# Performance work log

Hardware: AMD Instinct MI355X
Metric: run time of the kernel (lower is better)

## Reference

```python
import jax, jax.numpy as jnp
import numpy as np

TEMP = 0.5
ALPHA, BETA, GAMMA, LAMB = 1e-3, 5e-4, 1e-3, 5e-6
IMG = 1024.0  # img_metas img_shape (H_img, W_img)
LN_EPS = 1e-5


def setup_inputs() -> dict:
    key = jax.random.key(0)
    ks = jax.random.split(key, 20)
    N, C, H, W, NB = 8, 256, 128, 128, 20
    preds_S = jax.random.normal(ks[0], (N, C, H, W), jnp.float32)
    preds_T = jax.random.normal(ks[1], (N, C, H, W), jnp.float32)
    # valid boxes (tl_x, tl_y, br_x, br_y) in pixel coords within [0, IMG]
    raw = jax.random.uniform(ks[2], (N, NB, 4), jnp.float32)
    x1 = raw[..., 0] * 0.7 * IMG
    y1 = raw[..., 1] * 0.7 * IMG
    x2 = jnp.minimum(x1 + (0.05 + raw[..., 2] * 0.25) * IMG, IMG)
    y2 = jnp.minimum(y1 + (0.05 + raw[..., 3] * 0.25) * IMG, IMG)
    gt_bboxes = jnp.stack([x1, y1, x2, y2], axis=-1)
    s = 1.0 / np.sqrt(C)
    s2 = 1.0 / np.sqrt(C // 2)
    mk = lambda k, shape, sc: jax.random.normal(k, shape, jnp.float32) * sc
    return {
        'preds_S': preds_S, 'preds_T': preds_T, 'gt_bboxes': gt_bboxes,
        'w_ms': mk(ks[3], (C,), s), 'b_ms': jnp.zeros((), jnp.float32),
        'w_mt': mk(ks[4], (C,), s), 'b_mt': jnp.zeros((), jnp.float32),
        'w1_s': mk(ks[5], (C // 2, C), s), 'b1_s': jnp.zeros((C // 2,), jnp.float32),
        'g_s': jnp.ones((C // 2,), jnp.float32), 'be_s': jnp.zeros((C // 2,), jnp.float32),
        'w2_s': mk(ks[6], (C, C // 2), s2), 'b2_s': jnp.zeros((C,), jnp.float32),
        'w1_t': mk(ks[7], (C // 2, C), s), 'b1_t': jnp.zeros((C // 2,), jnp.float32),
        'g_t': jnp.ones((C // 2,), jnp.float32), 'be_t': jnp.zeros((C // 2,), jnp.float32),
        'w2_t': mk(ks[8], (C, C // 2), s2), 'b2_t': jnp.zeros((C,), jnp.float32),
    }


def _attention(x):
    # x: [N,C,H,W] -> S_att [N,H,W], C_att [N,C]
    N, C, H, W = x.shape
    v = jnp.abs(x)
    fea = v.mean(axis=1)                                   # [N,H,W]
    S = (H * W) * jax.nn.softmax((fea / TEMP).reshape(N, -1), axis=1)
    ch = v.mean(axis=(2, 3))                               # [N,C]
    Ca = C * jax.nn.softmax(ch / TEMP, axis=1)
    return S.reshape(N, H, W), Ca


def _masks(gt, H, W):
    # gt: [N,nb,4] pixel coords; box-rasterized scatter-max foreground mask
    wmin = jnp.floor(gt[..., 0] / IMG * W)
    wmax = jnp.ceil(gt[..., 2] / IMG * W)
    hmin = jnp.floor(gt[..., 1] / IMG * H)
    hmax = jnp.ceil(gt[..., 3] / IMG * H)
    area = 1.0 / ((hmax + 1.0 - hmin) * (wmax + 1.0 - wmin))  # [N,nb]
    hs = jnp.arange(H, dtype=jnp.float32)[None, None, :, None]
    ws = jnp.arange(W, dtype=jnp.float32)[None, None, None, :]
    inb = (hs >= hmin[:, :, None, None]) & (hs <= hmax[:, :, None, None]) \
        & (ws >= wmin[:, :, None, None]) & (ws <= wmax[:, :, None, None])
    Mask_fg = jnp.where(inb, area[:, :, None, None], 0.0).max(axis=1)  # [N,H,W]
    Mask_bg = jnp.where(Mask_fg > 0, 0.0, 1.0)
    sbg = Mask_bg.sum(axis=(1, 2), keepdims=True)
    Mask_bg = jnp.where(sbg > 0, Mask_bg / sbg, Mask_bg)
    return Mask_fg, Mask_bg


def _spatial_pool(x, w, b):
    N, C, H, W = x.shape
    cm = jnp.einsum('nchw,c->nhw', x, w) + b
    sm = jax.nn.softmax(cm.reshape(N, -1), axis=1).reshape(N, H, W)
    return jnp.einsum('nchw,nhw->nc', x, sm)               # [N,C]


def _channel_add(ctx, w1, b1, g, be, w2, b2):
    y = ctx @ w1.T + b1                                    # [N,C/2]
    m = y.mean(axis=1, keepdims=True)
    v = y.var(axis=1, keepdims=True)
    y = (y - m) / jnp.sqrt(v + LN_EPS) * g + be
    y = jax.nn.relu(y)
    return y @ w2.T + b2                                   # [N,C]


def reference(preds_S, preds_T, gt_bboxes, w_ms, b_ms, w_mt, b_mt,
              w1_s, b1_s, g_s, be_s, w2_s, b2_s,
              w1_t, b1_t, g_t, be_t, w2_t, b2_t):
    N, C, H, W = preds_S.shape
    S_t, C_t = _attention(preds_T)
    S_s, C_s = _attention(preds_S)
    Mask_fg, Mask_bg = _masks(gt_bboxes, H, W)
    # feature losses: (fg_s - fg_t) = (S - T) * sqrt(S_t)*sqrt(C_t)*sqrt(mask)
    wgt = jnp.sqrt(S_t)[:, None] * jnp.sqrt(C_t)[:, :, None, None]
    d = (preds_S - preds_T) * wgt
    fg_loss = jnp.sum((d * jnp.sqrt(Mask_fg)[:, None]) ** 2) / N
    bg_loss = jnp.sum((d * jnp.sqrt(Mask_bg)[:, None]) ** 2) / N
    mask_loss = jnp.sum(jnp.abs(C_s - C_t)) / N + jnp.sum(jnp.abs(S_s - S_t)) / N
    ctx_s = _spatial_pool(preds_S, w_ms, b_ms)
    ctx_t = _spatial_pool(preds_T, w_mt, b_mt)
    add_s = _channel_add(ctx_s, w1_s, b1_s, g_s, be_s, w2_s, b2_s)
    add_t = _channel_add(ctx_t, w1_t, b1_t, g_t, be_t, w2_t, b2_t)
    rd = (preds_S + add_s[:, :, None, None]) - (preds_T + add_t[:, :, None, None])
    rela_loss = jnp.sum(rd ** 2) / N
    return ALPHA * fg_loss + BETA * bg_loss + GAMMA * mask_loss + LAMB * rela_loss
```

## Files before the change

kernel.cpp:

```cpp
#include <hip/hip_runtime.h>
#include <math.h>

#define NN    8
#define CC    256
#define HWHW  16384
#define NBOX  20

constexpr float C_ALPHA = 1e-3f, C_BETA = 5e-4f, C_GAMMA = 1e-3f, C_LAMB = 5e-6f;
constexpr float C_LN_EPS = 1e-5f;

#define OFF_FEA_S   0
#define OFF_FEA_T   131072
#define OFF_CM_S    262144
#define OFF_CM_T    393216
#define OFF_MFG     524288
#define OFF_PCHS    655360
#define OFF_PCHT    786432
#define OFF_PD      917504
#define OFF_PCTXS   1048576
#define OFF_PCTXT   1179648
#define OFF_CATT    1310720
#define OFF_CTXS    1312768
#define OFF_CTXT    1314816
#define OFF_DSUM    1316864
#define OFF_STATS   1318912
#define OFF_MXP     1318976
#define OFF_ZP      1319488
#define OFF_BG      1320000
#define OFF_SCAL    1320008
#define OFF_Y       1320016
#define OFF_RELAP   1322064

__device__ __forceinline__ float dpp_wave_sum(float x) {
#define DPPADD(ctrl, rm) \
  x += __int_as_float(__builtin_amdgcn_update_dpp(0, __float_as_int(x), ctrl, rm, 0xf, true));
  DPPADD(0x111, 0xf)
  DPPADD(0x112, 0xf)
  DPPADD(0x114, 0xf)
  DPPADD(0x118, 0xf)
  DPPADD(0x142, 0xa)
  DPPADD(0x143, 0xc)
#undef DPPADD
  return x;
}

__device__ __forceinline__ float dpp_wave_max(float x) {
#define DPPMAX(ctrl, rm) { \
  int r_ = __builtin_amdgcn_update_dpp(__float_as_int(x), __float_as_int(x), ctrl, rm, 0xf, false); \
  x = fmaxf(x, __int_as_float(r_)); }
  DPPMAX(0x111, 0xf)
  DPPMAX(0x112, 0xf)
  DPPMAX(0x114, 0xf)
  DPPMAX(0x118, 0xf)
  DPPMAX(0x142, 0xa)
  DPPMAX(0x143, 0xc)
#undef DPPMAX
  return x;
}

__device__ __forceinline__ float block_sum256(float v, float* sm) {
  int tid = threadIdx.x;
  v = dpp_wave_sum(v);
  if ((tid & 63) == 63) sm[tid >> 6] = v;
  __syncthreads();
  float r = sm[0] + sm[1] + sm[2] + sm[3];
  __syncthreads();
  return r;
}

__device__ __forceinline__ float block_max256(float v, float* sm) {
  int tid = threadIdx.x;
  v = dpp_wave_max(v);
  if ((tid & 63) == 63) sm[tid >> 6] = v;
  __syncthreads();
  float r = fmaxf(fmaxf(sm[0], sm[1]), fmaxf(sm[2], sm[3]));
  __syncthreads();
  return r;
}

__global__ __launch_bounds__(512, 8) void k1_pass1(
    const float* __restrict__ S, const float* __restrict__ T,
    const float* __restrict__ w_ms, const float* __restrict__ w_mt,
    float* __restrict__ ws) {
  int tid = threadIdx.x;
  int lane = tid & 63, sl = tid >> 6;
  int pb = blockIdx.x, cs = blockIdx.y, n = blockIdx.z;
  int pix0 = pb * 256 + lane * 4;
  int ch0 = cs * 128 + sl * 16;

  __shared__ float l_wS[128], l_wT[128];
  __shared__ float f_feaS[256], f_feaT[256], f_cmS[256], f_cmT[256];
  __shared__ float l_chS[128], l_chT[128], l_D[128];
  __shared__ float l_sq[8];

  if (tid < 128) {
    l_wS[tid] = w_ms[cs * 128 + tid];
    l_wT[tid] = w_mt[cs * 128 + tid];
  }
  if (tid < 256) {
    f_feaS[tid] = 0.f; f_feaT[tid] = 0.f; f_cmS[tid] = 0.f; f_cmT[tid] = 0.f;
  }
  __syncthreads();

  const float* baseS = S + (size_t)(n * CC + ch0) * HWHW + pix0;
  const float* baseT = T + (size_t)(n * CC + ch0) * HWHW + pix0;

  float fSx = 0, fSy = 0, fSz = 0, fSw = 0;
  float fTx = 0, fTy = 0, fTz = 0, fTw = 0;
  float cSx = 0, cSy = 0, cSz = 0, cSw = 0;
  float cTx = 0, cTy = 0, cTz = 0, cTw = 0;
  float sq = 0.f;

#pragma unroll 2
  for (int c = 0; c < 16; c++) {
    float4 s4 = *(const float4*)(baseS + (size_t)c * HWHW);
    float4 t4 = *(const float4*)(baseT + (size_t)c * HWHW);
    float asx = fabsf(s4.x), asy = fabsf(s4.y), asz = fabsf(s4.z), asw = fabsf(s4.w);
    float atx = fabsf(t4.x), aty = fabsf(t4.y), atz = fabsf(t4.z), atw = fabsf(t4.w);
    fSx += asx; fSy += asy; fSz += asz; fSw += asw;
    fTx += atx; fTy += aty; fTz += atz; fTw += atw;
    float wS = l_wS[sl * 16 + c], wT = l_wT[sl * 16 + c];
    cSx = fmaf(s4.x, wS, cSx); cSy = fmaf(s4.y, wS, cSy);
    cSz = fmaf(s4.z, wS, cSz); cSw = fmaf(s4.w, wS, cSw);
    cTx = fmaf(t4.x, wT, cTx); cTy = fmaf(t4.y, wT, cTy);
    cTz = fmaf(t4.z, wT, cTz); cTw = fmaf(t4.w, wT, cTw);
    float dx = s4.x - t4.x, dy = s4.y - t4.y, dz = s4.z - t4.z, dw = s4.w - t4.w;
    sq = fmaf(dx, dx, sq); sq = fmaf(dy, dy, sq);
    sq = fmaf(dz, dz, sq); sq = fmaf(dw, dw, sq);
    float chS_p = (asx + asy) + (asz + asw);
    float chT_p = (atx + aty) + (atz + atw);
    float d_p   = (dx + dy) + (dz + dw);
    chS_p = dpp_wave_sum(chS_p);
    chT_p = dpp_wave_sum(chT_p);
    d_p   = dpp_wave_sum(d_p);
    if (lane == 63) {
      l_chS[sl * 16 + c] = chS_p;
      l_chT[sl * 16 + c] = chT_p;
      l_D[sl * 16 + c]   = d_p;
    }
  }

  atomicAdd(&f_feaS[lane * 4 + 0], fSx); atomicAdd(&f_feaS[lane * 4 + 1], fSy);
  atomicAdd(&f_feaS[lane * 4 + 2], fSz); atomicAdd(&f_feaS[lane * 4 + 3], fSw);
  atomicAdd(&f_feaT[lane * 4 + 0], fTx); atomicAdd(&f_feaT[lane * 4 + 1], fTy);
  atomicAdd(&f_feaT[lane * 4 + 2], fTz); atomicAdd(&f_feaT[lane * 4 + 3], fTw);
  atomicAdd(&f_cmS[lane * 4 + 0], cSx); atomicAdd(&f_cmS[lane * 4 + 1], cSy);
  atomicAdd(&f_cmS[lane * 4 + 2], cSz); atomicAdd(&f_cmS[lane * 4 + 3], cSw);
  atomicAdd(&f_cmT[lane * 4 + 0], cTx); atomicAdd(&f_cmT[lane * 4 + 1], cTy);
  atomicAdd(&f_cmT[lane * 4 + 2], cTz); atomicAdd(&f_cmT[lane * 4 + 3], cTw);

  sq = dpp_wave_sum(sq);
  if (lane == 63) l_sq[sl] = sq;
  __syncthreads();

  if (tid < 256) {
    int gp = n * HWHW + pb * 256 + tid;
    atomicAdd(&ws[OFF_FEA_S + gp], f_feaS[tid]);
    atomicAdd(&ws[OFF_FEA_T + gp], f_feaT[tid]);
    atomicAdd(&ws[OFF_CM_S + gp],  f_cmS[tid]);
    atomicAdd(&ws[OFF_CM_T + gp],  f_cmT[tid]);
  }
  if (tid < 128) {
    int bo = (n * CC + cs * 128 + tid) * 64 + pb;
    ws[OFF_PCHS + bo] = l_chS[tid];
    ws[OFF_PCHT + bo] = l_chT[tid];
    ws[OFF_PD + bo]   = l_D[tid];
  }
  if (tid == 0) {
    float t = 0.f;
#pragma unroll
    for (int i = 0; i < 8; i++) t += l_sq[i];
    atomicAdd(&ws[OFF_SCAL + 0], t);
  }
}

__global__ __launch_bounds__(256) void k2_mask(const float* __restrict__ gt,
                                               float* __restrict__ ws) {
  int tid = threadIdx.x;
  int n   = blockIdx.x >> 6;
  int pix = ((blockIdx.x & 63) << 8) | tid;
  float hf = (float)(pix >> 7), wf = (float)(pix & 127);

  __shared__ float bx[NBOX][5];
  __shared__ float l_bg[4];
  if (tid < NBOX) {
    const float* g = gt + (n * NBOX + tid) * 4;
    float wmin = floorf(g[0] * 0.125f);
    float hmin = floorf(g[1] * 0.125f);
    float wmax = ceilf(g[2] * 0.125f);
    float hmax = ceilf(g[3] * 0.125f);
    bx[tid][0] = wmin; bx[tid][1] = hmin; bx[tid][2] = wmax; bx[tid][3] = hmax;
    bx[tid][4] = 1.0f / ((hmax + 1.0f - hmin) * (wmax + 1.0f - wmin));
  }
  __syncthreads();

  float best = 0.f;
#pragma unroll
  for (int b = 0; b < NBOX; b++) {
    bool in = (hf >= bx[b][1]) && (hf <= bx[b][3]) && (wf >= bx[b][0]) && (wf <= bx[b][2]);
    best = in ? fmaxf(best, bx[b][4]) : best;
  }
  ws[OFF_MFG + n * HWHW + pix] = best;

  float bg = (best > 0.f) ? 0.f : 1.f;
  bg = dpp_wave_sum(bg);
  if ((tid & 63) == 63) l_bg[tid >> 6] = bg;
  __syncthreads();
  if (tid == 0) atomicAdd(&ws[OFF_BG + n], l_bg[0] + l_bg[1] + l_bg[2] + l_bg[3]);
}

__global__ __launch_bounds__(256) void kB_stats1(float* __restrict__ ws) {
  int tid = threadIdx.x;
  int pb = blockIdx.x, n = blockIdx.y;
  __shared__ float sm[4];
  int pix0 = pb * 1024 + tid * 4;
  const int   offs[4]   = {OFF_FEA_S, OFF_FEA_T, OFF_CM_S, OFF_CM_T};
  const float scales[4] = {1.0f / 128.0f, 1.0f / 128.0f, 1.0f, 1.0f};
#pragma unroll
  for (int a = 0; a < 4; a++) {
    float4 v = *(const float4*)&ws[offs[a] + n * HWHW + pix0];
    float sc = scales[a];
    v.x *= sc; v.y *= sc; v.z *= sc; v.w *= sc;
    float mx = fmaxf(fmaxf(v.x, v.y), fmaxf(v.z, v.w));
    mx = block_max256(mx, sm);
    float z = expf(v.x - mx) + expf(v.y - mx) + expf(v.z - mx) + expf(v.w - mx);
    z = block_sum256(z, sm);
    if (tid == 0) {
      ws[OFF_MXP + a * 128 + n * 16 + pb] = mx;
      ws[OFF_ZP + a * 128 + n * 16 + pb]  = z;
    }
  }
}

__global__ __launch_bounds__(256) void kC_stats2(float* __restrict__ ws) {
  int tid = threadIdx.x, n = blockIdx.x;
  __shared__ float sm[4];

  float chS = 0.f, chT = 0.f, Dv = 0.f;
  int base = (n * CC + tid) * 64;
#pragma unroll 4
  for (int k = 0; k < 64; k += 4) {
    float4 a = *(const float4*)&ws[OFF_PCHS + base + k];
    float4 b = *(const float4*)&ws[OFF_PCHT + base + k];
    float4 d = *(const float4*)&ws[OFF_PD + base + k];
    chS += (a.x + a.y) + (a.z + a.w);
    chT += (b.x + b.y) + (b.z + b.w);
    Dv  += (d.x + d.y) + (d.z + d.w);
  }
  ws[OFF_DSUM + n * CC + tid] = Dv;

  float lS = chS * (1.0f / 8192.0f), lT = chT * (1.0f / 8192.0f);
  float mS = block_max256(lS, sm);
  float mT = block_max256(lT, sm);
  float eS = expf(lS - mS), eT = expf(lT - mT);
  float ZS = block_sum256(eS, sm);
  float ZT = block_sum256(eT, sm);
  float cattS = (float)CC * eS / ZS;
  float cattT = (float)CC * eT / ZT;
  ws[OFF_CATT + n * CC + tid] = cattT;
  float mml = block_sum256(fabsf(cattS - cattT), sm);
  if (tid == 0) atomicAdd(&ws[OFF_SCAL + 2], mml);

  if (tid < 4) {
    int a = tid;
    float m = -1e30f;
    for (int i = 0; i < 16; i++)
      m = fmaxf(m, ws[OFF_MXP + a * 128 + n * 16 + i]);
    float Z = 0.f;
    for (int i = 0; i < 16; i++)
      Z += ws[OFF_ZP + a * 128 + n * 16 + i] *
           expf(ws[OFF_MXP + a * 128 + n * 16 + i] - m);
    ws[OFF_STATS + n * 8 + 2 * a]     = m;
    ws[OFF_STATS + n * 8 + 2 * a + 1] = Z;
  }
}

__global__ __launch_bounds__(512, 8) void k4_pass2(
    const float* __restrict__ S, const float* __restrict__ T,
    float* __restrict__ ws) {
  int tid = threadIdx.x;
  int lane = tid & 63, sl = tid >> 6;
  int pb = blockIdx.x, cs = blockIdx.y, n = blockIdx.z;
  int pix0 = pb * 256 + lane * 4;
  int ch0 = cs * 128 + sl * 16;

  __shared__ float l_catt[128];
  __shared__ float wcombL[256], smsL[256], smtL[256];
  __shared__ float l_cs[128], l_ct[128], l_c[8];

  if (tid < 128) l_catt[tid] = ws[OFF_CATT + n * CC + cs * 128 + tid];
  if (tid < 64) {
    float mxFS = ws[OFF_STATS + n * 8 + 0], ZFS = ws[OFF_STATS + n * 8 + 1];
    float mxFT = ws[OFF_STATS + n * 8 + 2], ZFT = ws[OFF_STATS + n * 8 + 3];
    float mxCS = ws[OFF_STATS + n * 8 + 4], ZCS = ws[OFF_STATS + n * 8 + 5];
    float mxCT = ws[OFF_STATS + n * 8 + 6], ZCT = ws[OFF_STATS + n * 8 + 7];
    float bgc  = ws[OFF_BG + n];
    int gp = n * HWHW + pb * 256 + tid * 4;
    float4 fS = *(const float4*)&ws[OFF_FEA_S + gp];
    float4 fT = *(const float4*)&ws[OFF_FEA_T + gp];
    float4 cS = *(const float4*)&ws[OFF_CM_S + gp];
    float4 cT = *(const float4*)&ws[OFF_CM_T + gp];
    float4 mf = *(const float4*)&ws[OFF_MFG + gp];
    float macc = 0.f;
    float fSa[4] = {fS.x, fS.y, fS.z, fS.w};
    float fTa[4] = {fT.x, fT.y, fT.z, fT.w};
    float cSa[4] = {cS.x, cS.y, cS.z, cS.w};
    float cTa[4] = {cT.x, cT.y, cT.z, cT.w};
    float mfa[4] = {mf.x, mf.y, mf.z, mf.w};
#pragma unroll
    for (int j = 0; j < 4; j++) {
      float pT = expf(fTa[j] * (1.0f / 128.0f) - mxFT) / ZFT;
      float pS = expf(fSa[j] * (1.0f / 128.0f) - mxFS) / ZFS;
      float Satt = (float)HWHW * pT;
      float mbg = (mfa[j] > 0.f) ? 0.f : ((bgc > 0.f) ? 1.0f / bgc : 1.0f);
      wcombL[tid * 4 + j] = Satt * (C_ALPHA * mfa[j] + C_BETA * mbg);
      smsL[tid * 4 + j] = expf(cSa[j] - mxCS) / ZCS;
      smtL[tid * 4 + j] = expf(cTa[j] - mxCT) / ZCT;
      macc += fabsf(pS - pT);
    }
    macc = dpp_wave_sum(macc);
    if (tid == 63 && cs == 0) atomicAdd(&ws[OFF_SCAL + 2], macc * (float)HWHW);
  }
  __syncthreads();

  float4 sms = *(const float4*)&smsL[lane * 4];
  float4 smt = *(const float4*)&smtL[lane * 4];
  float4 wcb = *(const float4*)&wcombL[lane * 4];

  const float* baseS = S + (size_t)(n * CC + ch0) * HWHW + pix0;
  const float* baseT = T + (size_t)(n * CC + ch0) * HWHW + pix0;

  float awx = 0, awy = 0, awz = 0, aww = 0;
#pragma unroll 2
  for (int c = 0; c < 16; c++) {
    float4 s4 = *(const float4*)(baseS + (size_t)c * HWHW);
    float4 t4 = *(const float4*)(baseT + (size_t)c * HWHW);
    float ca = l_catt[sl * 16 + c];
    float dx = s4.x - t4.x, dy = s4.y - t4.y, dz = s4.z - t4.z, dw = s4.w - t4.w;
    awx = fmaf(dx * dx, ca, awx); awy = fmaf(dy * dy, ca, awy);
    awz = fmaf(dz * dz, ca, awz); aww = fmaf(dw * dw, ca, aww);
    float xs = fmaf(s4.x, sms.x, fmaf(s4.y, sms.y, fmaf(s4.z, sms.z, s4.w * sms.w)));
    float xt = fmaf(t4.x, smt.x, fmaf(t4.y, smt.y, fmaf(t4.z, smt.z, t4.w * smt.w)));
    xs = dpp_wave_sum(xs);
    xt = dpp_wave_sum(xt);
    if (lane == 63) { l_cs[sl * 16 + c] = xs; l_ct[sl * 16 + c] = xt; }
  }

  float contrib = fmaf(awx, wcb.x, fmaf(awy, wcb.y, fmaf(awz, wcb.z, aww * wcb.w)));
  contrib = dpp_wave_sum(contrib);
  if (lane == 63) l_c[sl] = contrib;
  __syncthreads();

  if (tid < 128) {
    int bo = (n * CC + cs * 128 + tid) * 64 + pb;
    ws[OFF_PCTXS + bo] = l_cs[tid];
    ws[OFF_PCTXT + bo] = l_ct[tid];
  }
  if (tid == 0) {
    float t = 0.f;
#pragma unroll
    for (int i = 0; i < 8; i++) t += l_c[i];
    atomicAdd(&ws[OFF_SCAL + 1], t);
  }
}

__global__ __launch_bounds__(256) void k4b_ctxreduce(float* __restrict__ ws) {
  int tid = threadIdx.x, n = blockIdx.x;
  float a = 0.f, b = 0.f;
  int base = (n * CC + tid) * 64;
#pragma unroll 4
  for (int k = 0; k < 64; k += 4) {
    float4 x = *(const float4*)&ws[OFF_PCTXS + base + k];
    float4 y = *(const float4*)&ws[OFF_PCTXT + base + k];
    a += (x.x + x.y) + (x.z + x.w);
    b += (y.x + y.y) + (y.z + y.w);
  }
  ws[OFF_CTXS + n * CC + tid] = a;
  ws[OFF_CTXT + n * CC + tid] = b;
}

__global__ __launch_bounds__(128) void k5a_mlp1(
    const float* __restrict__ w1_s, const float* __restrict__ b1_s,
    const float* __restrict__ g_s,  const float* __restrict__ be_s,
    const float* __restrict__ w1_t, const float* __restrict__ b1_t,
    const float* __restrict__ g_t,  const float* __restrict__ be_t,
    float* __restrict__ ws) {
  int tid = threadIdx.x;
  int n = blockIdx.x >> 1, st = blockIdx.x & 1;
  const float* w1 = st ? w1_t : w1_s;
  const float* b1 = st ? b1_t : b1_s;
  const float* g  = st ? g_t  : g_s;
  const float* be = st ? be_t : be_s;
  int ctxoff = (st ? OFF_CTXT : OFF_CTXS) + n * CC;

  __shared__ float ctx[CC];
  __shared__ float red[2];
  ctx[tid]       = ws[ctxoff + tid];
  ctx[tid + 128] = ws[ctxoff + tid + 128];
  __syncthreads();

  float acc = b1[tid];
  const float* wr = w1 + tid * CC;
#pragma unroll 8
  for (int c = 0; c < CC; c += 4) {
    float4 w = *(const float4*)(wr + c);
    acc = fmaf(w.x, ctx[c], acc);
    acc = fmaf(w.y, ctx[c + 1], acc);
    acc = fmaf(w.z, ctx[c + 2], acc);
    acc = fmaf(w.w, ctx[c + 3], acc);
  }

  float v = dpp_wave_sum(acc);
  if ((tid & 63) == 63) red[tid >> 6] = v;
  __syncthreads();
  float mean = (red[0] + red[1]) * (1.0f / 128.0f);
  __syncthreads();
  float dm = acc - mean;
  v = dpp_wave_sum(dm * dm);
  if ((tid & 63) == 63) red[tid >> 6] = v;
  __syncthreads();
  float var = (red[0] + red[1]) * (1.0f / 128.0f);
  float q = dm * (1.0f / sqrtf(var + C_LN_EPS)) * g[tid] + be[tid];
  ws[OFF_Y + blockIdx.x * 128 + tid] = q > 0.f ? q : 0.f;
}

__global__ __launch_bounds__(256) void k5b_mlp2(
    const float* __restrict__ w2_s, const float* __restrict__ b2_s,
    const float* __restrict__ w2_t, const float* __restrict__ b2_t,
    float* __restrict__ ws) {
  int tid = threadIdx.x, n = blockIdx.x;
  __shared__ float ysh[128], yth[128];
  __shared__ float sm[4];
  if (tid < 128) ysh[tid] = ws[OFF_Y + (n * 2 + 0) * 128 + tid];
  else           yth[tid - 128] = ws[OFF_Y + (n * 2 + 1) * 128 + (tid - 128)];
  __syncthreads();

  float es = b2_s[tid], et = b2_t[tid];
  const float* w2sr = w2_s + tid * 128;
  const float* w2tr = w2_t + tid * 128;
#pragma unroll 8
  for (int j = 0; j < 128; j += 4) {
    float4 a = *(const float4*)(w2sr + j);
    float4 b = *(const float4*)(w2tr + j);
    es = fmaf(a.x, ysh[j], es); es = fmaf(a.y, ysh[j + 1], es);
    es = fmaf(a.z, ysh[j + 2], es); es = fmaf(a.w, ysh[j + 3], es);
    et = fmaf(b.x, yth[j], et); et = fmaf(b.y, yth[j + 1], et);
    et = fmaf(b.z, yth[j + 2], et); et = fmaf(b.w, yth[j + 3], et);
  }
  float e = es - et;
  float rp = 2.0f * e * ws[OFF_DSUM + n * CC + tid] + (float)HWHW * e * e;
  rp = block_sum256(rp, sm);
  if (tid == 0) ws[OFF_RELAP + n] = rp;
}

__global__ __launch_bounds__(64) void k5c_final(float* __restrict__ ws,
                                                float* __restrict__ out) {
  int lane = threadIdx.x;
  float r = (lane < NN) ? ws[OFF_RELAP + lane] : 0.f;
  r = dpp_wave_sum(r);
  if (lane == 63) {
    float rela = ws[OFF_SCAL + 0] + r;
    out[0] = (ws[OFF_SCAL + 1] + C_GAMMA * ws[OFF_SCAL + 2] + C_LAMB * rela) *
             (1.0f / (float)NN);
  }
}

extern "C" void kernel_launch(void* const* d_in, const int* in_sizes, int n_in,
                              void* d_out, int out_size, void* d_ws, size_t ws_size,
                              hipStream_t stream) {
  const float* S    = (const float*)d_in[0];
  const float* T    = (const float*)d_in[1];
  const float* gt   = (const float*)d_in[2];
  const float* w_ms = (const float*)d_in[3];
  const float* w_mt = (const float*)d_in[5];
  const float* w1_s = (const float*)d_in[7];
  const float* b1_s = (const float*)d_in[8];
  const float* g_s  = (const float*)d_in[9];
  const float* be_s = (const float*)d_in[10];
  const float* w2_s = (const float*)d_in[11];
  const float* b2_s = (const float*)d_in[12];
  const float* w1_t = (const float*)d_in[13];
  const float* b1_t = (const float*)d_in[14];
  const float* g_t  = (const float*)d_in[15];
  const float* be_t = (const float*)d_in[16];
  const float* w2_t = (const float*)d_in[17];
  const float* b2_t = (const float*)d_in[18];
  float* ws = (float*)d_ws;
  float* out = (float*)d_out;

  hipMemsetAsync(ws, 0, 524288 * sizeof(float), stream);
  hipMemsetAsync(ws + OFF_BG, 0, 16 * sizeof(float), stream);

  k1_pass1<<<dim3(64, 2, 8), dim3(512), 0, stream>>>(S, T, w_ms, w_mt, ws);
  k2_mask<<<dim3(512), dim3(256), 0, stream>>>(gt, ws);
  kB_stats1<<<dim3(16, 8), dim3(256), 0, stream>>>(ws);
  kC_stats2<<<dim3(8), dim3(256), 0, stream>>>(ws);
  k4_pass2<<<dim3(64, 2, 8), dim3(512), 0, stream>>>(S, T, ws);
  k4b_ctxreduce<<<dim3(8), dim3(256), 0, stream>>>(ws);
  k5a_mlp1<<<dim3(16), dim3(128), 0, stream>>>(w1_s, b1_s, g_s, be_s,
                                               w1_t, b1_t, g_t, be_t, ws);
  k5b_mlp2<<<dim3(8), dim3(256), 0, stream>>>(w2_s, b2_s, w2_t, b2_t, ws);
  k5c_final<<<dim3(1), dim3(64), 0, stream>>>(ws, out);
}
```

Measured before the change: 447.7 us.

## Fuse mask and softmax stats kernels, shrink pass blocks, prefetch channel loads

New measurement: 798.0 us. +78.3%, slower.

```diff
diff --git a/kernel.cpp b/kernel.cpp
--- a/kernel.cpp
+++ b/kernel.cpp
@@ -20,16 +20,10 @@
 #define OFF_PCTXS   1048576
 #define OFF_PCTXT   1179648
 #define OFF_CATT    1310720
-#define OFF_CTXS    1312768
-#define OFF_CTXT    1314816
-#define OFF_DSUM    1316864
-#define OFF_STATS   1318912
-#define OFF_MXP     1318976
-#define OFF_ZP      1319488
-#define OFF_BG      1320000
-#define OFF_SCAL    1320008
-#define OFF_Y       1320016
-#define OFF_RELAP   1322064
+#define OFF_DSUM    1312768
+#define OFF_SCAL    1314816
+#define OFF_Y       1314824
+#define OFF_RELAP   1316872
 
 __device__ __forceinline__ float dpp_wave_sum(float x) {
 #define DPPADD(ctrl, rm) \
@@ -58,6 +52,29 @@
   return x;
 }
 
+__device__ __forceinline__ float blk_sum16(float v, float* scr) {
+  int tid = threadIdx.x;
+  v = dpp_wave_sum(v);
+  if ((tid & 63) == 63) scr[tid >> 6] = v;
+  __syncthreads();
+  float r = 0.f;
+#pragma unroll
+  for (int i = 0; i < 16; i++) r += scr[i];
+  __syncthreads();
+  return r;
+}
+__device__ __forceinline__ float blk_max16(float v, float* scr) {
+  int tid = threadIdx.x;
+  v = dpp_wave_max(v);
+  if ((tid & 63) == 63) scr[tid >> 6] = v;
+  __syncthreads();
+  float r = -1e30f;
+#pragma unroll
+  for (int i = 0; i < 16; i++) r = fmaxf(r, scr[i]);
+  __syncthreads();
+  return r;
+}
+
 __device__ __forceinline__ float block_sum256(float v, float* sm) {
   int tid = threadIdx.x;
   v = dpp_wave_sum(v);
@@ -68,121 +85,113 @@
   return r;
 }
 
-__device__ __forceinline__ float block_max256(float v, float* sm) {
-  int tid = threadIdx.x;
-  v = dpp_wave_max(v);
-  if ((tid & 63) == 63) sm[tid >> 6] = v;
-  __syncthreads();
-  float r = fmaxf(fmaxf(sm[0], sm[1]), fmaxf(sm[2], sm[3]));
-  __syncthreads();
-  return r;
-}
-
-__global__ __launch_bounds__(512, 8) void k1_pass1(
+__global__ __launch_bounds__(256, 8) void k1_pass1(
     const float* __restrict__ S, const float* __restrict__ T,
     const float* __restrict__ w_ms, const float* __restrict__ w_mt,
     float* __restrict__ ws) {
   int tid = threadIdx.x;
-  int lane = tid & 63, sl = tid >> 6;
-  int pb = blockIdx.x, cs = blockIdx.y, n = blockIdx.z;
+  int lane = tid & 63, wv = tid >> 6;
+  int pb = blockIdx.x, cq = blockIdx.y, n = blockIdx.z;
   int pix0 = pb * 256 + lane * 4;
-  int ch0 = cs * 128 + sl * 16;
-
-  __shared__ float l_wS[128], l_wT[128];
+  int ch0 = cq * 64 + wv * 16;
+
+  __shared__ float l_wS[64], l_wT[64];
   __shared__ float f_feaS[256], f_feaT[256], f_cmS[256], f_cmT[256];
-  __shared__ float l_chS[128], l_chT[128], l_D[128];
-  __shared__ float l_sq[8];
-
-  if (tid < 128) {
-    l_wS[tid] = w_ms[cs * 128 + tid];
-    l_wT[tid] = w_mt[cs * 128 + tid];
-  }
-  if (tid < 256) {
-    f_feaS[tid] = 0.f; f_feaT[tid] = 0.f; f_cmS[tid] = 0.f; f_cmT[tid] = 0.f;
-  }
+  __shared__ float l_chS[64], l_chT[64], l_D[64];
+  __shared__ float l_sq[4];
+
+  if (tid < 64) {
+    l_wS[tid] = w_ms[cq * 64 + tid];
+    l_wT[tid] = w_mt[cq * 64 + tid];
+  }
+  f_feaS[tid] = 0.f; f_feaT[tid] = 0.f; f_cmS[tid] = 0.f; f_cmT[tid] = 0.f;
   __syncthreads();
 
   const float* baseS = S + (size_t)(n * CC + ch0) * HWHW + pix0;
   const float* baseT = T + (size_t)(n * CC + ch0) * HWHW + pix0;
 
-  float fSx = 0, fSy = 0, fSz = 0, fSw = 0;
-  float fTx = 0, fTy = 0, fTz = 0, fTw = 0;
-  float cSx = 0, cSy = 0, cSz = 0, cSw = 0;
-  float cTx = 0, cTy = 0, cTz = 0, cTw = 0;
+  float fS0 = 0, fS1 = 0, fS2 = 0, fS3 = 0;
+  float fT0 = 0, fT1 = 0, fT2 = 0, fT3 = 0;
+  float cS0 = 0, cS1 = 0, cS2 = 0, cS3 = 0;
+  float cT0 = 0, cT1 = 0, cT2 = 0, cT3 = 0;
   float sq = 0.f;
 
-#pragma unroll 2
-  for (int c = 0; c < 16; c++) {
-    float4 s4 = *(const float4*)(baseS + (size_t)c * HWHW);
-    float4 t4 = *(const float4*)(baseT + (size_t)c * HWHW);
-    float asx = fabsf(s4.x), asy = fabsf(s4.y), asz = fabsf(s4.z), asw = fabsf(s4.w);
-    float atx = fabsf(t4.x), aty = fabsf(t4.y), atz = fabsf(t4.z), atw = fabsf(t4.w);
-    fSx += asx; fSy += asy; fSz += asz; fSw += asw;
-    fTx += atx; fTy += aty; fTz += atz; fTw += atw;
-    float wS = l_wS[sl * 16 + c], wT = l_wT[sl * 16 + c];
-    cSx = fmaf(s4.x, wS, cSx); cSy = fmaf(s4.y, wS, cSy);
-    cSz = fmaf(s4.z, wS, cSz); cSw = fmaf(s4.w, wS, cSw);
-    cTx = fmaf(t4.x, wT, cTx); cTy = fmaf(t4.y, wT, cTy);
-    cTz = fmaf(t4.z, wT, cTz); cTw = fmaf(t4.w, wT, cTw);
-    float dx = s4.x - t4.x, dy = s4.y - t4.y, dz = s4.z - t4.z, dw = s4.w - t4.w;
-    sq = fmaf(dx, dx, sq); sq = fmaf(dy, dy, sq);
-    sq = fmaf(dz, dz, sq); sq = fmaf(dw, dw, sq);
-    float chS_p = (asx + asy) + (asz + asw);
-    float chT_p = (atx + aty) + (atz + atw);
-    float d_p   = (dx + dy) + (dz + dw);
-    chS_p = dpp_wave_sum(chS_p);
-    chT_p = dpp_wave_sum(chT_p);
-    d_p   = dpp_wave_sum(d_p);
-    if (lane == 63) {
-      l_chS[sl * 16 + c] = chS_p;
-      l_chT[sl * 16 + c] = chT_p;
-      l_D[sl * 16 + c]   = d_p;
+#define PROC1(s4, t4, cc_) { \
+  float asx = fabsf(s4.x), asy = fabsf(s4.y), asz = fabsf(s4.z), asw = fabsf(s4.w); \
+  float atx = fabsf(t4.x), aty = fabsf(t4.y), atz = fabsf(t4.z), atw = fabsf(t4.w); \
+  fS0 += asx; fS1 += asy; fS2 += asz; fS3 += asw; \
+  fT0 += atx; fT1 += aty; fT2 += atz; fT3 += atw; \
+  float wS = l_wS[wv * 16 + (cc_)], wT = l_wT[wv * 16 + (cc_)]; \
+  cS0 = fmaf(s4.x, wS, cS0); cS1 = fmaf(s4.y, wS, cS1); \
+  cS2 = fmaf(s4.z, wS, cS2); cS3 = fmaf(s4.w, wS, cS3); \
+  cT0 = fmaf(t4.x, wT, cT0); cT1 = fmaf(t4.y, wT, cT1); \
+  cT2 = fmaf(t4.z, wT, cT2); cT3 = fmaf(t4.w, wT, cT3); \
+  float dx = s4.x - t4.x, dy = s4.y - t4.y, dz = s4.z - t4.z, dw = s4.w - t4.w; \
+  sq = fmaf(dx, dx, sq); sq = fmaf(dy, dy, sq); \
+  sq = fmaf(dz, dz, sq); sq = fmaf(dw, dw, sq); \
+  float cp = (asx + asy) + (asz + asw); \
+  float tp = (atx + aty) + (atz + atw); \
+  float dp = (dx + dy) + (dz + dw); \
+  cp = dpp_wave_sum(cp); tp = dpp_wave_sum(tp); dp = dpp_wave_sum(dp); \
+  if (lane == 63) { l_chS[wv * 16 + (cc_)] = cp; l_chT[wv * 16 + (cc_)] = tp; \
+                    l_D[wv * 16 + (cc_)] = dp; } }
+
+  float4 sA = *(const float4*)(baseS);
+  float4 tA = *(const float4*)(baseT);
+  float4 sB = *(const float4*)(baseS + HWHW);
+  float4 tB = *(const float4*)(baseT + HWHW);
+#pragma unroll
+  for (int p = 0; p < 8; p++) {
+    float4 s0 = sA, t0 = tA, s1 = sB, t1 = tB;
+    if (p < 7) {
+      const float* qS = baseS + (size_t)(2 * p + 2) * HWHW;
+      const float* qT = baseT + (size_t)(2 * p + 2) * HWHW;
+      sA = *(const float4*)(qS);
+      tA = *(const float4*)(qT);
+      sB = *(const float4*)(qS + HWHW);
+      tB = *(const float4*)(qT + HWHW);
     }
-  }
-
-  atomicAdd(&f_feaS[lane * 4 + 0], fSx); atomicAdd(&f_feaS[lane * 4 + 1], fSy);
-  atomicAdd(&f_feaS[lane * 4 + 2], fSz); atomicAdd(&f_feaS[lane * 4 + 3], fSw);
-  atomicAdd(&f_feaT[lane * 4 + 0], fTx); atomicAdd(&f_feaT[lane * 4 + 1], fTy);
-  atomicAdd(&f_feaT[lane * 4 + 2], fTz); atomicAdd(&f_feaT[lane * 4 + 3], fTw);
-  atomicAdd(&f_cmS[lane * 4 + 0], cSx); atomicAdd(&f_cmS[lane * 4 + 1], cSy);
-  atomicAdd(&f_cmS[lane * 4 + 2], cSz); atomicAdd(&f_cmS[lane * 4 + 3], cSw);
-  atomicAdd(&f_cmT[lane * 4 + 0], cTx); atomicAdd(&f_cmT[lane * 4 + 1], cTy);
-  atomicAdd(&f_cmT[lane * 4 + 2], cTz); atomicAdd(&f_cmT[lane * 4 + 3], cTw);
+    PROC1(s0, t0, 2 * p)
+    PROC1(s1, t1, 2 * p + 1)
+  }
+#undef PROC1
+
+  atomicAdd(&f_feaS[lane * 4 + 0], fS0); atomicAdd(&f_feaS[lane * 4 + 1], fS1);
+  atomicAdd(&f_feaS[lane * 4 + 2], fS2); atomicAdd(&f_feaS[lane * 4 + 3], fS3);
+  atomicAdd(&f_feaT[lane * 4 + 0], fT0); atomicAdd(&f_feaT[lane * 4 + 1], fT1);
+  atomicAdd(&f_feaT[lane * 4 + 2], fT2); atomicAdd(&f_feaT[lane * 4 + 3], fT3);
+  atomicAdd(&f_cmS[lane * 4 + 0], cS0); atomicAdd(&f_cmS[lane * 4 + 1], cS1);
+  atomicAdd(&f_cmS[lane * 4 + 2], cS2); atomicAdd(&f_cmS[lane * 4 + 3], cS3);
+  atomicAdd(&f_cmT[lane * 4 + 0], cT0); atomicAdd(&f_cmT[lane * 4 + 1], cT1);
+  atomicAdd(&f_cmT[lane * 4 + 2], cT2); atomicAdd(&f_cmT[lane * 4 + 3], cT3);
 
   sq = dpp_wave_sum(sq);
-  if (lane == 63) l_sq[sl] = sq;
-  __syncthreads();
-
-  if (tid < 256) {
-    int gp = n * HWHW + pb * 256 + tid;
-    atomicAdd(&ws[OFF_FEA_S + gp], f_feaS[tid]);
-    atomicAdd(&ws[OFF_FEA_T + gp], f_feaT[tid]);
-    atomicAdd(&ws[OFF_CM_S + gp],  f_cmS[tid]);
-    atomicAdd(&ws[OFF_CM_T + gp],  f_cmT[tid]);
-  }
-  if (tid < 128) {
-    int bo = (n * CC + cs * 128 + tid) * 64 + pb;
+  if (lane == 63) l_sq[wv] = sq;
+  __syncthreads();
+
+  int gp = n * HWHW + pb * 256 + tid;
+  atomicAdd(&ws[OFF_FEA_S + gp], f_feaS[tid]);
+  atomicAdd(&ws[OFF_FEA_T + gp], f_feaT[tid]);
+  atomicAdd(&ws[OFF_CM_S + gp],  f_cmS[tid]);
+  atomicAdd(&ws[OFF_CM_T + gp],  f_cmT[tid]);
+
+  if (tid < 64) {
+    int bo = (n * CC + cq * 64 + tid) * 64 + pb;
     ws[OFF_PCHS + bo] = l_chS[tid];
     ws[OFF_PCHT + bo] = l_chT[tid];
     ws[OFF_PD + bo]   = l_D[tid];
   }
-  if (tid == 0) {
-    float t = 0.f;
-#pragma unroll
-    for (int i = 0; i < 8; i++) t += l_sq[i];
-    atomicAdd(&ws[OFF_SCAL + 0], t);
-  }
-}
-
-__global__ __launch_bounds__(256) void k2_mask(const float* __restrict__ gt,
+  if (tid == 0)
+    atomicAdd(&ws[OFF_SCAL + 0], l_sq[0] + l_sq[1] + l_sq[2] + l_sq[3]);
+}
+
+__global__ __launch_bounds__(1024) void k3_mid(const float* __restrict__ gt,
                                                float* __restrict__ ws) {
-  int tid = threadIdx.x;
-  int n   = blockIdx.x >> 6;
-  int pix = ((blockIdx.x & 63) << 8) | tid;
-  float hf = (float)(pix >> 7), wf = (float)(pix & 127);
-
+  int tid = threadIdx.x, n = blockIdx.x;
   __shared__ float bx[NBOX][5];
-  __shared__ float l_bg[4];
+  __shared__ float scr[16];
+  __shared__ float l_cpart[3][4][256];
+
   if (tid < NBOX) {
     const float* g = gt + (n * NBOX + tid) * 4;
     float wmin = floorf(g[0] * 0.125f);
@@ -194,189 +203,215 @@
   }
   __syncthreads();
 
-  float best = 0.f;
-#pragma unroll
-  for (int b = 0; b < NBOX; b++) {
-    bool in = (hf >= bx[b][1]) && (hf <= bx[b][3]) && (wf >= bx[b][0]) && (wf <= bx[b][2]);
-    best = in ? fmaxf(best, bx[b][4]) : best;
-  }
-  ws[OFF_MFG + n * HWHW + pix] = best;
-
-  float bg = (best > 0.f) ? 0.f : 1.f;
-  bg = dpp_wave_sum(bg);
-  if ((tid & 63) == 63) l_bg[tid >> 6] = bg;
-  __syncthreads();
-  if (tid == 0) atomicAdd(&ws[OFF_BG + n], l_bg[0] + l_bg[1] + l_bg[2] + l_bg[3]);
-}
-
-__global__ __launch_bounds__(256) void kB_stats1(float* __restrict__ ws) {
-  int tid = threadIdx.x;
-  int pb = blockIdx.x, n = blockIdx.y;
-  __shared__ float sm[4];
-  int pix0 = pb * 1024 + tid * 4;
-  const int   offs[4]   = {OFF_FEA_S, OFF_FEA_T, OFF_CM_S, OFF_CM_T};
-  const float scales[4] = {1.0f / 128.0f, 1.0f / 128.0f, 1.0f, 1.0f};
-#pragma unroll
-  for (int a = 0; a < 4; a++) {
-    float4 v = *(const float4*)&ws[offs[a] + n * HWHW + pix0];
-    float sc = scales[a];
-    v.x *= sc; v.y *= sc; v.z *= sc; v.w *= sc;
-    float mx = fmaxf(fmaxf(v.x, v.y), fmaxf(v.z, v.w));
-    mx = block_max256(mx, sm);
-    float z = expf(v.x - mx) + expf(v.y - mx) + expf(v.z - mx) + expf(v.w - mx);
-    z = block_sum256(z, sm);
-    if (tid == 0) {
-      ws[OFF_MXP + a * 128 + n * 16 + pb] = mx;
-      ws[OFF_ZP + a * 128 + n * 16 + pb]  = z;
+  float mxFS = -1e30f, mxFT = -1e30f, mxCS = -1e30f, mxCT = -1e30f;
+  float bg = 0.f;
+#pragma unroll
+  for (int s = 0; s < 4; s++) {
+    int pix = (tid + s * 1024) * 4;
+    float hf = (float)(pix >> 7);
+    float wf = (float)(pix & 127);
+    float b0 = 0, b1 = 0, b2 = 0, b3 = 0;
+#pragma unroll
+    for (int b = 0; b < NBOX; b++) {
+      if (hf >= bx[b][1] && hf <= bx[b][3]) {
+        float wmn = bx[b][0], wmx = bx[b][2], ar = bx[b][4];
+        if (wf >= wmn && wf <= wmx) b0 = fmaxf(b0, ar);
+        if (wf + 1.f >= wmn && wf + 1.f <= wmx) b1 = fmaxf(b1, ar);
+        if (wf + 2.f >= wmn && wf + 2.f <= wmx) b2 = fmaxf(b2, ar);
+        if (wf + 3.f >= wmn && wf + 3.f <= wmx) b3 = fmaxf(b3, ar);
+      }
     }
-  }
-}
-
-__global__ __launch_bounds__(256) void kC_stats2(float* __restrict__ ws) {
-  int tid = threadIdx.x, n = blockIdx.x;
-  __shared__ float sm[4];
-
-  float chS = 0.f, chT = 0.f, Dv = 0.f;
-  int base = (n * CC + tid) * 64;
-#pragma unroll 4
-  for (int k = 0; k < 64; k += 4) {
-    float4 a = *(const float4*)&ws[OFF_PCHS + base + k];
-    float4 b = *(const float4*)&ws[OFF_PCHT + base + k];
-    float4 d = *(const float4*)&ws[OFF_PD + base + k];
-    chS += (a.x + a.y) + (a.z + a.w);
-    chT += (b.x + b.y) + (b.z + b.w);
-    Dv  += (d.x + d.y) + (d.z + d.w);
-  }
-  ws[OFF_DSUM + n * CC + tid] = Dv;
-
-  float lS = chS * (1.0f / 8192.0f), lT = chT * (1.0f / 8192.0f);
-  float mS = block_max256(lS, sm);
-  float mT = block_max256(lT, sm);
-  float eS = expf(lS - mS), eT = expf(lT - mT);
-  float ZS = block_sum256(eS, sm);
-  float ZT = block_sum256(eT, sm);
-  float cattS = (float)CC * eS / ZS;
-  float cattT = (float)CC * eT / ZT;
-  ws[OFF_CATT + n * CC + tid] = cattT;
-  float mml = block_sum256(fabsf(cattS - cattT), sm);
+    *(float4*)&ws[OFF_MFG + n * HWHW + pix] = make_float4(b0, b1, b2, b3);
+    bg += (b0 > 0 ? 0.f : 1.f) + (b1 > 0 ? 0.f : 1.f) +
+          (b2 > 0 ? 0.f : 1.f) + (b3 > 0 ? 0.f : 1.f);
+    float4 fS = *(const float4*)&ws[OFF_FEA_S + n * HWHW + pix];
+    float4 fT = *(const float4*)&ws[OFF_FEA_T + n * HWHW + pix];
+    float4 cS = *(const float4*)&ws[OFF_CM_S + n * HWHW + pix];
+    float4 cT = *(const float4*)&ws[OFF_CM_T + n * HWHW + pix];
+    mxFS = fmaxf(mxFS, fmaxf(fmaxf(fS.x, fS.y), fmaxf(fS.z, fS.w)));
+    mxFT = fmaxf(mxFT, fmaxf(fmaxf(fT.x, fT.y), fmaxf(fT.z, fT.w)));
+    mxCS = fmaxf(mxCS, fmaxf(fmaxf(cS.x, cS.y), fmaxf(cS.z, cS.w)));
+    mxCT = fmaxf(mxCT, fmaxf(fmaxf(cT.x, cT.y), fmaxf(cT.z, cT.w)));
+  }
+  bg = blk_sum16(bg, scr);
+  float invbg = (bg > 0.f) ? 1.0f / bg : 1.0f;
+  mxFS = blk_max16(mxFS, scr) * (1.0f / 128.0f);
+  mxFT = blk_max16(mxFT, scr) * (1.0f / 128.0f);
+  mxCS = blk_max16(mxCS, scr);
+  mxCT = blk_max16(mxCT, scr);
+
+  float zFS = 0, zFT = 0, zCS = 0, zCT = 0;
+#pragma unroll
+  for (int s = 0; s < 4; s++) {
+    int pix = (tid + s * 1024) * 4;
+    float4 fS = *(const float4*)&ws[OFF_FEA_S + n * HWHW + pix];
+    float4 fT = *(const float4*)&ws[OFF_FEA_T + n * HWHW + pix];
+    float4 cS = *(const float4*)&ws[OFF_CM_S + n * HWHW + pix];
+    float4 cT = *(const float4*)&ws[OFF_CM_T + n * HWHW + pix];
+    zFS += expf(fS.x * (1.f/128.f) - mxFS) + expf(fS.y * (1.f/128.f) - mxFS)
+         + expf(fS.z * (1.f/128.f) - mxFS) + expf(fS.w * (1.f/128.f) - mxFS);
+    zFT += expf(fT.x * (1.f/128.f) - mxFT) + expf(fT.y * (1.f/128.f) - mxFT)
+         + expf(fT.z * (1.f/128.f) - mxFT) + expf(fT.w * (1.f/128.f) - mxFT);
+    zCS += expf(cS.x - mxCS) + expf(cS.y - mxCS) + expf(cS.z - mxCS) + expf(cS.w - mxCS);
+    zCT += expf(cT.x - mxCT) + expf(cT.y - mxCT) + expf(cT.z - mxCT) + expf(cT.w - mxCT);
+  }
+  zFS = blk_sum16(zFS, scr);
+  zFT = blk_sum16(zFT, scr);
+  zCS = blk_sum16(zCS, scr);
+  zCT = blk_sum16(zCT, scr);
+  float iZFS = 1.0f / zFS, iZFT = 1.0f / zFT, iZCS = 1.0f / zCS, iZCT = 1.0f / zCT;
+
+  float macc = 0.f;
+#pragma unroll
+  for (int s = 0; s < 4; s++) {
+    int pix = (tid + s * 1024) * 4;
+    float4 fS = *(const float4*)&ws[OFF_FEA_S + n * HWHW + pix];
+    float4 fT = *(const float4*)&ws[OFF_FEA_T + n * HWHW + pix];
+    float4 cS = *(const float4*)&ws[OFF_CM_S + n * HWHW + pix];
+    float4 cT = *(const float4*)&ws[OFF_CM_T + n * HWHW + pix];
+    float4 mf = *(const float4*)&ws[OFF_MFG + n * HWHW + pix];
+    float4 wc, sms, smt;
+    float pS, pT, mbg;
+#define PXC(j, fs_, ft_, cs_, ct_, mf_) \
+    pT = expf(ft_ * (1.f/128.f) - mxFT) * iZFT; \
+    pS = expf(fs_ * (1.f/128.f) - mxFS) * iZFS; \
+    macc += fabsf(pS - pT); \
+    mbg = (mf_ > 0.f) ? 0.f : invbg; \
+    wc.j = (float)HWHW * pT * (C_ALPHA * mf_ + C_BETA * mbg); \
+    sms.j = expf(cs_ - mxCS) * iZCS; \
+    smt.j = expf(ct_ - mxCT) * iZCT;
+    PXC(x, fS.x, fT.x, cS.x, cT.x, mf.x)
+    PXC(y, fS.y, fT.y, cS.y, cT.y, mf.y)
+    PXC(z, fS.z, fT.z, cS.z, cT.z, mf.z)
+    PXC(w, fS.w, fT.w, cS.w, cT.w, mf.w)
+#undef PXC
+    *(float4*)&ws[OFF_FEA_T + n * HWHW + pix] = wc;
+    *(float4*)&ws[OFF_CM_S + n * HWHW + pix]  = sms;
+    *(float4*)&ws[OFF_CM_T + n * HWHW + pix]  = smt;
+  }
+  macc = blk_sum16(macc, scr);
+  if (tid == 0) atomicAdd(&ws[OFF_SCAL + 2], macc * (float)HWHW);
+
+  int c = tid & 255, qg = tid >> 8;
+  float aS = 0, aT = 0, aD = 0;
+  int cb = (n * CC + c) * 64 + qg * 16;
+#pragma unroll
+  for (int k = 0; k < 16; k += 4) {
+    float4 x = *(const float4*)&ws[OFF_PCHS + cb + k];
+    float4 y = *(const float4*)&ws[OFF_PCHT + cb + k];
+    float4 z = *(const float4*)&ws[OFF_PD + cb + k];
+    aS += (x.x + x.y) + (x.z + x.w);
+    aT += (y.x + y.y) + (y.z + y.w);
+    aD += (z.x + z.y) + (z.z + z.w);
+  }
+  l_cpart[0][qg][c] = aS;
+  l_cpart[1][qg][c] = aT;
+  l_cpart[2][qg][c] = aD;
+  __syncthreads();
+
+  bool act = tid < 256;
+  float lS = -1e30f, lT = -1e30f;
+  if (act) {
+    float chS = l_cpart[0][0][tid] + l_cpart[0][1][tid] + l_cpart[0][2][tid] + l_cpart[0][3][tid];
+    float chT = l_cpart[1][0][tid] + l_cpart[1][1][tid] + l_cpart[1][2][tid] + l_cpart[1][3][tid];
+    float Dv  = l_cpart[2][0][tid] + l_cpart[2][1][tid] + l_cpart[2][2][tid] + l_cpart[2][3][tid];
+    ws[OFF_DSUM + n * CC + tid] = Dv;
+    lS = chS * (1.0f / 8192.0f);
+    lT = chT * (1.0f / 8192.0f);
+  }
+  float mS = blk_max16(lS, scr);
+  float mT = blk_max16(lT, scr);
+  float eS = act ? expf(lS - mS) : 0.f;
+  float eT = act ? expf(lT - mT) : 0.f;
+  float ZS = blk_sum16(eS, scr);
+  float ZT = blk_sum16(eT, scr);
+  float mml = 0.f;
+  if (act) {
+    float cattS = (float)CC * eS / ZS;
+    float cattT = (float)CC * eT / ZT;
+    ws[OFF_CATT + n * CC + tid] = cattT;
+    mml = fabsf(cattS - cattT);
+  }
+  mml = blk_sum16(mml, scr);
   if (tid == 0) atomicAdd(&ws[OFF_SCAL + 2], mml);
-
-  if (tid < 4) {
-    int a = tid;
-    float m = -1e30f;
-    for (int i = 0; i < 16; i++)
-      m = fmaxf(m, ws[OFF_MXP + a * 128 + n * 16 + i]);
-    float Z = 0.f;
-    for (int i = 0; i < 16; i++)
-      Z += ws[OFF_ZP + a * 128 + n * 16 + i] *
-           expf(ws[OFF_MXP + a * 128 + n * 16 + i] - m);
-    ws[OFF_STATS + n * 8 + 2 * a]     = m;
-    ws[OFF_STATS + n * 8 + 2 * a + 1] = Z;
-  }
-}
-
-__global__ __launch_bounds__(512, 8) void k4_pass2(
+}
+
+__global__ __launch_bounds__(256, 8) void k4_pass2(
     const float* __restrict__ S, const float* __restrict__ T,
     float* __restrict__ ws) {
   int tid = threadIdx.x;
-  int lane = tid & 63, sl = tid >> 6;
-  int pb = blockIdx.x, cs = blockIdx.y, n = blockIdx.z;
+  int lane = tid & 63, wv = tid >> 6;
+  int pb = blockIdx.x, cq = blockIdx.y, n = blockIdx.z;
   int pix0 = pb * 256 + lane * 4;
-  int ch0 = cs * 128 + sl * 16;
-
-  __shared__ float l_catt[128];
+  int ch0 = cq * 64 + wv * 16;
+
+  __shared__ float l_catt[64];
   __shared__ float wcombL[256], smsL[256], smtL[256];
-  __shared__ float l_cs[128], l_ct[128], l_c[8];
-
-  if (tid < 128) l_catt[tid] = ws[OFF_CATT + n * CC + cs * 128 + tid];
+  __shared__ float l_cs[64], l_ct[64], l_c[4];
+
   if (tid < 64) {
-    float mxFS = ws[OFF_STATS + n * 8 + 0], ZFS = ws[OFF_STATS + n * 8 + 1];
-    float mxFT = ws[OFF_STATS + n * 8 + 2], ZFT = ws[OFF_STATS + n * 8 + 3];
-    float mxCS = ws[OFF_STATS + n * 8 + 4], ZCS = ws[OFF_STATS + n * 8 + 5];
-    float mxCT = ws[OFF_STATS + n * 8 + 6], ZCT = ws[OFF_STATS + n * 8 + 7];
-    float bgc  = ws[OFF_BG + n];
+    l_catt[tid] = ws[OFF_CATT + n * CC + cq * 64 + tid];
     int gp = n * HWHW + pb * 256 + tid * 4;
-    float4 fS = *(const float4*)&ws[OFF_FEA_S + gp];
-    float4 fT = *(const float4*)&ws[OFF_FEA_T + gp];
-    float4 cS = *(const float4*)&ws[OFF_CM_S + gp];
-    float4 cT = *(const float4*)&ws[OFF_CM_T + gp];
-    float4 mf = *(const float4*)&ws[OFF_MFG + gp];
-    float macc = 0.f;
-    float fSa[4] = {fS.x, fS.y, fS.z, fS.w};
-    float fTa[4] = {fT.x, fT.y, fT.z, fT.w};
-    float cSa[4] = {cS.x, cS.y, cS.z, cS.w};
-    float cTa[4] = {cT.x, cT.y, cT.z, cT.w};
-    float mfa[4] = {mf.x, mf.y, mf.z, mf.w};
-#pragma unroll
-    for (int j = 0; j < 4; j++) {
-      float pT = expf(fTa[j] * (1.0f / 128.0f) - mxFT) / ZFT;
-      float pS = expf(fSa[j] * (1.0f / 128.0f) - mxFS) / ZFS;
-      float Satt = (float)HWHW * pT;
-      float mbg = (mfa[j] > 0.f) ? 0.f : ((bgc > 0.f) ? 1.0f / bgc : 1.0f);
-      wcombL[tid * 4 + j] = Satt * (C_ALPHA * mfa[j] + C_BETA * mbg);
-      smsL[tid * 4 + j] = expf(cSa[j] - mxCS) / ZCS;
-      smtL[tid * 4 + j] = expf(cTa[j] - mxCT) / ZCT;
-      macc += fabsf(pS - pT);
-    }
-    macc = dpp_wave_sum(macc);
-    if (tid == 63 && cs == 0) atomicAdd(&ws[OFF_SCAL + 2], macc * (float)HWHW);
-  }
-  __syncthreads();
-
-  float4 sms = *(const float4*)&smsL[lane * 4];
-  float4 smt = *(const float4*)&smtL[lane * 4];
-  float4 wcb = *(const float4*)&wcombL[lane * 4];
+    float4 wc = *(const float4*)&ws[OFF_FEA_T + gp];
+    float4 a  = *(const float4*)&ws[OFF_CM_S + gp];
+    float4 b  = *(const float4*)&ws[OFF_CM_T + gp];
+    *(float4*)&wcombL[tid * 4] = wc;
+    *(float4*)&smsL[tid * 4]   = a;
+    *(float4*)&smtL[tid * 4]   = b;
+  }
+  __syncthreads();
+
+  float4 sms4 = *(const float4*)&smsL[lane * 4];
+  float4 smt4 = *(const float4*)&smtL[lane * 4];
+  float4 wcb  = *(const float4*)&wcombL[lane * 4];
 
   const float* baseS = S + (size_t)(n * CC + ch0) * HWHW + pix0;
   const float* baseT = T + (size_t)(n * CC + ch0) * HWHW + pix0;
 
-  float awx = 0, awy = 0, awz = 0, aww = 0;
-#pragma unroll 2
-  for (int c = 0; c < 16; c++) {
-    float4 s4 = *(const float4*)(baseS + (size_t)c * HWHW);
-    float4 t4 = *(const float4*)(baseT + (size_t)c * HWHW);
-    float ca = l_catt[sl * 16 + c];
-    float dx = s4.x - t4.x, dy = s4.y - t4.y, dz = s4.z - t4.z, dw = s4.w - t4.w;
-    awx = fmaf(dx * dx, ca, awx); awy = fmaf(dy * dy, ca, awy);
-    awz = fmaf(dz * dz, ca, awz); aww = fmaf(dw * dw, ca, aww);
-    float xs = fmaf(s4.x, sms.x, fmaf(s4.y, sms.y, fmaf(s4.z, sms.z, s4.w * sms.w)));
-    float xt = fmaf(t4.x, smt.x, fmaf(t4.y, smt.y, fmaf(t4.z, smt.z, t4.w * smt.w)));
-    xs = dpp_wave_sum(xs);
-    xt = dpp_wave_sum(xt);
-    if (lane == 63) { l_cs[sl * 16 + c] = xs; l_ct[sl * 16 + c] = xt; }
-  }
-
-  float contrib = fmaf(awx, wcb.x, fmaf(awy, wcb.y, fmaf(awz, wcb.z, aww * wcb.w)));
+  float aw0 = 0, aw1 = 0, aw2 = 0, aw3 = 0;
+
+#define PROC4(s4, t4, cc_) { \
+  float ca = l_catt[wv * 16 + (cc_)]; \
+  float dx = s4.x - t4.x, dy = s4.y - t4.y, dz = s4.z - t4.z, dw = s4.w - t4.w; \
+  aw0 = fmaf(dx * dx, ca, aw0); aw1 = fmaf(dy * dy, ca, aw1); \
+  aw2 = fmaf(dz * dz, ca, aw2); aw3 = fmaf(dw * dw, ca, aw3); \
+  float xs = fmaf(s4.x, sms4.x, fmaf(s4.y, sms4.y, fmaf(s4.z, sms4.z, s4.w * sms4.w))); \
+  float xt = fmaf(t4.x, smt4.x, fmaf(t4.y, smt4.y, fmaf(t4.z, smt4.z, t4.w * smt4.w))); \
+  xs = dpp_wave_sum(xs); xt = dpp_wave_sum(xt); \
+  if (lane == 63) { l_cs[wv * 16 + (cc_)] = xs; l_ct[wv * 16 + (cc_)] = xt; } }
+
+  float4 sA = *(const float4*)(baseS);
+  float4 tA = *(const float4*)(baseT);
+  float4 sB = *(const float4*)(baseS + HWHW);
+  float4 tB = *(const float4*)(baseT + HWHW);
+#pragma unroll
+  for (int p = 0; p < 8; p++) {
+    float4 s0 = sA, t0 = tA, s1 = sB, t1 = tB;
+    if (p < 7) {
+      const float* qS = baseS + (size_t)(2 * p + 2) * HWHW;
+      const float* qT = baseT + (size_t)(2 * p + 2) * HWHW;
+      sA = *(const float4*)(qS);
+      tA = *(const float4*)(qT);
+      sB = *(const float4*)(qS + HWHW);
+      tB = *(const float4*)(qT + HWHW);
+    }
+    PROC4(s0, t0, 2 * p)
+    PROC4(s1, t1, 2 * p + 1)
+  }
+#undef PROC4
+
+  float contrib = fmaf(aw0, wcb.x, fmaf(aw1, wcb.y, fmaf(aw2, wcb.z, aw3 * wcb.w)));
   contrib = dpp_wave_sum(contrib);
-  if (lane == 63) l_c[sl] = contrib;
-  __syncthreads();
-
-  if (tid < 128) {
-    int bo = (n * CC + cs * 128 + tid) * 64 + pb;
+  if (lane == 63) l_c[wv] = contrib;
+  __syncthreads();
+
+  if (tid < 64) {
+    int bo = (n * CC + cq * 64 + tid) * 64 + pb;
     ws[OFF_PCTXS + bo] = l_cs[tid];
     ws[OFF_PCTXT + bo] = l_ct[tid];
   }
-  if (tid == 0) {
-    float t = 0.f;
-#pragma unroll
-    for (int i = 0; i < 8; i++) t += l_c[i];
-    atomicAdd(&ws[OFF_SCAL + 1], t);
-  }
-}
-
-__global__ __launch_bounds__(256) void k4b_ctxreduce(float* __restrict__ ws) {
-  int tid = threadIdx.x, n = blockIdx.x;
-  float a = 0.f, b = 0.f;
-  int base = (n * CC + tid) * 64;
-#pragma unroll 4
-  for (int k = 0; k < 64; k += 4) {
-    float4 x = *(const float4*)&ws[OFF_PCTXS + base + k];
-    float4 y = *(const float4*)&ws[OFF_PCTXT + base + k];
-    a += (x.x + x.y) + (x.z + x.w);
-    b += (y.x + y.y) + (y.z + y.w);
-  }
-  ws[OFF_CTXS + n * CC + tid] = a;
-  ws[OFF_CTXT + n * CC + tid] = b;
+  if (tid == 0)
+    atomicAdd(&ws[OFF_SCAL + 1], l_c[0] + l_c[1] + l_c[2] + l_c[3]);
 }
 
 __global__ __launch_bounds__(128) void k5a_mlp1(
@@ -391,12 +426,20 @@
   const float* b1 = st ? b1_t : b1_s;
   const float* g  = st ? g_t  : g_s;
   const float* be = st ? be_t : be_s;
-  int ctxoff = (st ? OFF_CTXT : OFF_CTXS) + n * CC;
+  int poff = st ? OFF_PCTXT : OFF_PCTXS;
 
   __shared__ float ctx[CC];
   __shared__ float red[2];
-  ctx[tid]       = ws[ctxoff + tid];
-  ctx[tid + 128] = ws[ctxoff + tid + 128];
+  for (int c = tid; c < CC; c += 128) {
+    float a = 0.f;
+    int base = poff + (n * CC + c) * 64;
+#pragma unroll
+    for (int k = 0; k < 64; k += 4) {
+      float4 x = *(const float4*)&ws[base + k];
+      a += (x.x + x.y) + (x.z + x.w);
+    }
+    ctx[c] = a;
+  }
   __syncthreads();
 
   float acc = b1[tid];
@@ -489,14 +532,11 @@
   float* out = (float*)d_out;
 
   hipMemsetAsync(ws, 0, 524288 * sizeof(float), stream);
-  hipMemsetAsync(ws + OFF_BG, 0, 16 * sizeof(float), stream);
-
-  k1_pass1<<<dim3(64, 2, 8), dim3(512), 0, stream>>>(S, T, w_ms, w_mt, ws);
-  k2_mask<<<dim3(512), dim3(256), 0, stream>>>(gt, ws);
-  kB_stats1<<<dim3(16, 8), dim3(256), 0, stream>>>(ws);
-  kC_stats2<<<dim3(8), dim3(256), 0, stream>>>(ws);
-  k4_pass2<<<dim3(64, 2, 8), dim3(512), 0, stream>>>(S, T, ws);
-  k4b_ctxreduce<<<dim3(8), dim3(256), 0, stream>>>(ws);
+  hipMemsetAsync(ws + OFF_SCAL, 0, 8 * sizeof(float), stream);
+
+  k1_pass1<<<dim3(64, 4, 8), dim3(256), 0, stream>>>(S, T, w_ms, w_mt, ws);
+  k3_mid<<<dim3(8), dim3(1024), 0, stream>>>(gt, ws);
+  k4_pass2<<<dim3(64, 4, 8), dim3(256), 0, stream>>>(S, T, ws);
   k5a_mlp1<<<dim3(16), dim3(128), 0, stream>>>(w1_s, b1_s, g_s, be_s,
                                                w1_t, b1_t, g_t, be_t, ws);
   k5b_mlp2<<<dim3(8), dim3(256), 0, stream>>>(w2_s, b2_s, w2_t, b2_t, ws);
```
